# Kernel tuning notes

Hardware: AMD Instinct MI355X
Metric: run time of the kernel (lower is better)

The kernel has to match this reference:

```python
import jax, jax.numpy as jnp
import numpy as np

N_GRAPHS = 256
NEG_SLOPE = 0.2


def _add_self_loops(src, dst, edge_attr, n):
    # PyG fill_value='mean': self-loop edge_attr = per-node mean of incoming edge_attr
    sums = jax.ops.segment_sum(edge_attr, dst, num_segments=n)
    cnt = jax.ops.segment_sum(jnp.ones((dst.shape[0],), edge_attr.dtype), dst, num_segments=n)
    loop_attr = sums / jnp.maximum(cnt, 1.0)[:, None]
    loop = jnp.arange(n)
    src = jnp.concatenate([src, loop])
    dst = jnp.concatenate([dst, loop])
    ea = jnp.concatenate([edge_attr, loop_attr], axis=0)
    return src, dst, ea


def _segment_softmax(scores, seg, n):
    # scores: [E, H]; softmax over edges sharing the same target node
    m = jax.ops.segment_max(scores, seg, num_segments=n)
    ex = jnp.exp(scores - m[seg])
    s = jax.ops.segment_sum(ex, seg, num_segments=n)
    return ex / jnp.maximum(s[seg], 1e-16)


def gatv2_layer(x, src, dst, ea, w_l, w_r, w_e, att, b, heads, out_ch, concat):
    n = x.shape[0]
    x_l = (x @ w_l).reshape(n, heads, out_ch)  # source transform
    x_r = (x @ w_r).reshape(n, heads, out_ch)  # target transform
    e_f = (ea @ w_e).reshape(-1, heads, out_ch)
    m = x_l[src] + x_r[dst] + e_f                               # [E, H, C]
    score = jnp.einsum('ehc,hc->eh', jax.nn.leaky_relu(m, NEG_SLOPE), att)
    alpha = _segment_softmax(score, dst, n)                      # [E, H]
    out = jax.ops.segment_sum(alpha[:, :, None] * x_l[src], dst, num_segments=n)
    if concat:
        return out.reshape(n, heads * out_ch) + b
    return out.mean(axis=1) + b


def reference(x, edge_index, edge_attr, batch,
              w_l1, w_r1, w_e1, att1, b1,
              w_l2, w_r2, w_e2, att2, b2,
              w_fc, b_fc):
    n = x.shape[0]
    src, dst, ea = _add_self_loops(edge_index[0], edge_index[1], edge_attr, n)
    h = gatv2_layer(x, src, dst, ea, w_l1, w_r1, w_e1, att1, b1, heads=2, out_ch=32, concat=True)
    h = jax.nn.relu(h)
    h = gatv2_layer(h, src, dst, ea, w_l2, w_r2, w_e2, att2, b2, heads=1, out_ch=32, concat=False)
    h = jax.nn.relu(h)
    # global mean pool over graphs
    sums = jax.ops.segment_sum(h, batch, num_segments=N_GRAPHS)
    cnt = jax.ops.segment_sum(jnp.ones((n,), h.dtype), batch, num_segments=N_GRAPHS)
    pooled = sums / jnp.maximum(cnt, 1.0)[:, None]
    return pooled @ w_fc + b_fc


def setup_inputs() -> dict:
    key = jax.random.key(0)
    ks = jax.random.split(key, 20)
    N, E, IN, H, C, ED, OUT = 100000, 1600000, 128, 2, 32, 16, 32
    s = 0.05
    return {
        'x': jax.random.normal(ks[0], (N, IN), jnp.float32),
        'edge_index': jax.random.randint(ks[1], (2, E), 0, N, jnp.int32),
        'edge_attr': jax.random.normal(ks[2], (E, ED), jnp.float32),
        'batch': jnp.sort(jax.random.randint(ks[3], (N,), 0, 256, jnp.int32)),
        'w_l1': jax.random.normal(ks[4], (IN, H * C), jnp.float32) * s,
        'w_r1': jax.random.normal(ks[5], (IN, H * C), jnp.float32) * s,
        'w_e1': jax.random.normal(ks[6], (ED, H * C), jnp.float32) * s,
        'att1': jax.random.normal(ks[7], (H, C), jnp.float32) * s,
        'b1': jnp.zeros((H * C,), jnp.float32),
        'w_l2': jax.random.normal(ks[8], (H * C, C), jnp.float32) * s,
        'w_r2': jax.random.normal(ks[9], (H * C, C), jnp.float32) * s,
        'w_e2': jax.random.normal(ks[10], (ED, C), jnp.float32) * s,
        'att2': jax.random.normal(ks[11], (1, C), jnp.float32) * s,
        'b2': jnp.zeros((C,), jnp.float32),
        'w_fc': jax.random.normal(ks[12], (C, OUT), jnp.float32) * s,
        'b_fc': jnp.zeros((OUT,), jnp.float32),
    }
```

## Files before the change

kernel.cpp:

```cpp
#include <hip/hip_runtime.h>
#include <hip/hip_bf16.h>
#include <hip/hip_fp16.h>

#define NEG_SLOPE 0.2f
#define LOG2E 1.4426950408889634f
#define NROUNDS 8

typedef _Float16 h2v __attribute__((ext_vector_type(2)));
typedef __fp16 f16x2 __attribute__((ext_vector_type(2)));
union hu { h2v h; f16x2 f; unsigned int u; };

__device__ __forceinline__ float dot16h(uint4 u0, uint4 u1, const h2v* wh) {
  union { uint4 u; h2v h[4]; } a0, a1;
  a0.u = u0; a1.u = u1;
  float f0 = 0.f, f1 = 0.f;
  f0 = __builtin_amdgcn_fdot2(a0.h[0], wh[0], f0, false);
  f1 = __builtin_amdgcn_fdot2(a0.h[1], wh[1], f1, false);
  f0 = __builtin_amdgcn_fdot2(a0.h[2], wh[2], f0, false);
  f1 = __builtin_amdgcn_fdot2(a0.h[3], wh[3], f1, false);
  f0 = __builtin_amdgcn_fdot2(a1.h[0], wh[4], f0, false);
  f1 = __builtin_amdgcn_fdot2(a1.h[1], wh[5], f1, false);
  f0 = __builtin_amdgcn_fdot2(a1.h[2], wh[6], f0, false);
  f1 = __builtin_amdgcn_fdot2(a1.h[3], wh[7], f1, false);
  return f0 + f1;
}

__global__ void deg_count_k(const int* __restrict__ dstA, int* __restrict__ deg, int E) {
  int base = blockIdx.x * 1024 + threadIdx.x;
#pragma unroll
  for (int k = 0; k < 4; ++k) {
    int e = base + k * 256;
    if (e < E) atomicAdd(&deg[dstA[e]], 1);
  }
}

__global__ void scan1_k(const int* __restrict__ deg, int* __restrict__ rowptr,
                        int* __restrict__ aux, int N) {
  __shared__ int sh[256];
  int t = threadIdx.x, i = blockIdx.x * 256 + t;
  int v = (i < N) ? deg[i] : 0;
  sh[t] = v; __syncthreads();
  for (int off = 1; off < 256; off <<= 1) {
    int x = (t >= off) ? sh[t - off] : 0;
    __syncthreads();
    sh[t] += x;
    __syncthreads();
  }
  if (i < N) rowptr[i] = sh[t] - v;
  if (t == 255) aux[blockIdx.x] = sh[255];
}

__global__ void scan2_k(int* __restrict__ aux, int naux) {
  __shared__ int sh[512];
  int t = threadIdx.x;
  int v = (t < naux) ? aux[t] : 0;
  sh[t] = v; __syncthreads();
  for (int off = 1; off < 512; off <<= 1) {
    int x = (t >= off) ? sh[t - off] : 0;
    __syncthreads();
    sh[t] += x;
    __syncthreads();
  }
  if (t < naux) aux[t] = sh[t] - v;
}

__global__ void scan3_k(int* __restrict__ rowptr, int* __restrict__ cursor,
                        const int* __restrict__ aux, int N, int E) {
  int i = blockIdx.x * blockDim.x + threadIdx.x;
  if (i < N) {
    int r = rowptr[i] + aux[i >> 8];
    rowptr[i] = r;
    cursor[i] = r;
  } else if (i == N) {
    rowptr[N] = E;
  }
}

__global__ __launch_bounds__(256) void permute_ea_k(
    const int2* __restrict__ csr_se, const float* __restrict__ ea,
    unsigned int* __restrict__ ea_h_u, int E) {
  int gid = blockIdx.x * 256 + threadIdx.x;
  int slot = gid >> 3, sub = gid & 7;
  if (slot >= E) return;
  int eid = csr_se[slot].y;
  float2 v = ((const float2*)(ea + (size_t)eid * 16))[sub];
  hu p; p.f = __builtin_amdgcn_cvt_pkrtz(v.x, v.y);
  ea_h_u[(size_t)slot * 8 + sub] = p.u;
}

__global__ __launch_bounds__(256) void t1scat_k(
    const float* __restrict__ x, const float* __restrict__ wl, const float* __restrict__ wr,
    float* __restrict__ xl, float* __restrict__ xr, int N, int ntiles1,
    const int* __restrict__ srcA, const int* __restrict__ dstA,
    int* __restrict__ cursor, int2* __restrict__ csr_se, int E) {
  __shared__ unsigned int wS[64 * 128];
  __shared__ unsigned int xs[32 * 64];
  int t = threadIdx.x;
  if ((int)blockIdx.x >= ntiles1) {
    int sb = blockIdx.x - ntiles1;
    int round = sb & (NROUNDS - 1);
    int rb = sb >> 3;
    int nlo = (int)(((long long)round * N) / NROUNDS);
    int nhi = (int)(((long long)(round + 1) * N) / NROUNDS);
    int e4 = (rb * 256 + t) * 4;
    if (e4 + 3 < E) {
      int4 d4 = *(const int4*)(dstA + e4);
      int4 s4 = *(const int4*)(srcA + e4);
#pragma unroll
      for (int k = 0; k < 4; ++k) {
        int d = (&d4.x)[k];
        if (d >= nlo && d < nhi) {
          int pos = atomicAdd(&cursor[d], 1);
          csr_se[pos] = make_int2((&s4.x)[k], e4 + k);
        }
      }
    } else {
      for (int k = 0; k < 4; ++k) {
        int e = e4 + k;
        if (e < E) {
          int d = dstA[e];
          if (d >= nlo && d < nhi) {
            int pos = atomicAdd(&cursor[d], 1);
            csr_se[pos] = make_int2(srcA[e], e);
          }
        }
      }
    }
    return;
  }
  int tile = blockIdx.x;
  for (int i = t; i < 64 * 64; i += 256) {
    int kp = i >> 6, j = i & 63;
    hu pl, pr;
    pl.f = __builtin_amdgcn_cvt_pkrtz(wl[(2 * kp) * 64 + j], wl[(2 * kp + 1) * 64 + j]);
    pr.f = __builtin_amdgcn_cvt_pkrtz(wr[(2 * kp) * 64 + j], wr[(2 * kp + 1) * 64 + j]);
    wS[kp * 128 + j]      = pl.u;
    wS[kp * 128 + 64 + j] = pr.u;
  }
  {
    int base = tile << 5;
    const float4* x4 = (const float4*)x;
    for (int i = t; i < 1024; i += 256) {
      int node = base + (i >> 5);
      float4 v = {0.f, 0.f, 0.f, 0.f};
      if (node < N) v = x4[(size_t)node * 32 + (i & 31)];
      hu p0, p1;
      p0.f = __builtin_amdgcn_cvt_pkrtz(v.x, v.y);
      p1.f = __builtin_amdgcn_cvt_pkrtz(v.z, v.w);
      uint2* d = (uint2*)&xs[(i >> 5) * 64 + (i & 31) * 2];
      *d = make_uint2(p0.u, p1.u);
    }
    __syncthreads();
    int tc = t & 31;
    int tr = t >> 5;
    float4 acc0 = {0,0,0,0}, acc1 = {0,0,0,0}, acc2 = {0,0,0,0}, acc3 = {0,0,0,0};
    const unsigned int* xrow = &xs[tr * 4 * 64];
#pragma unroll 4
    for (int kp = 0; kp < 64; ++kp) {
      uint4 wu = *(const uint4*)&wS[kp * 128 + tc * 4];
      hu w0, w1, w2, w3, q0, q1, q2, q3;
      w0.u = wu.x; w1.u = wu.y; w2.u = wu.z; w3.u = wu.w;
      q0.u = xrow[kp]; q1.u = xrow[64 + kp]; q2.u = xrow[128 + kp]; q3.u = xrow[192 + kp];
      acc0.x = __builtin_amdgcn_fdot2(q0.h, w0.h, acc0.x, false);
      acc0.y = __builtin_amdgcn_fdot2(q0.h, w1.h, acc0.y, false);
      acc0.z = __builtin_amdgcn_fdot2(q0.h, w2.h, acc0.z, false);
      acc0.w = __builtin_amdgcn_fdot2(q0.h, w3.h, acc0.w, false);
      acc1.x = __builtin_amdgcn_fdot2(q1.h, w0.h, acc1.x, false);
      acc1.y = __builtin_amdgcn_fdot2(q1.h, w1.h, acc1.y, false);
      acc1.z = __builtin_amdgcn_fdot2(q1.h, w2.h, acc1.z, false);
      acc1.w = __builtin_amdgcn_fdot2(q1.h, w3.h, acc1.w, false);
      acc2.x = __builtin_amdgcn_fdot2(q2.h, w0.h, acc2.x, false);
      acc2.y = __builtin_amdgcn_fdot2(q2.h, w1.h, acc2.y, false);
      acc2.z = __builtin_amdgcn_fdot2(q2.h, w2.h, acc2.z, false);
      acc2.w = __builtin_amdgcn_fdot2(q2.h, w3.h, acc2.w, false);
      acc3.x = __builtin_amdgcn_fdot2(q3.h, w0.h, acc3.x, false);
      acc3.y = __builtin_amdgcn_fdot2(q3.h, w1.h, acc3.y, false);
      acc3.z = __builtin_amdgcn_fdot2(q3.h, w2.h, acc3.z, false);
      acc3.w = __builtin_amdgcn_fdot2(q3.h, w3.h, acc3.w, false);
    }
    float* dp = (tc < 16) ? xl : xr;
    int j4 = (tc & 15) * 4;
    int nb = base + tr * 4;
    if (nb + 0 < N) *(float4*)&dp[(size_t)(nb + 0) * 64 + j4] = acc0;
    if (nb + 1 < N) *(float4*)&dp[(size_t)(nb + 1) * 64 + j4] = acc1;
    if (nb + 2 < N) *(float4*)&dp[(size_t)(nb + 2) * 64 + j4] = acc2;
    if (nb + 3 < N) *(float4*)&dp[(size_t)(nb + 3) * 64 + j4] = acc3;
  }
}

__global__ __launch_bounds__(256) void transform2_k(
    const float* __restrict__ h, const float* __restrict__ wl, const float* __restrict__ wr,
    float* __restrict__ xl, float* __restrict__ xr, int N) {
  __shared__ unsigned int wS[32 * 64];
  __shared__ unsigned int xs[64 * 32];
  int t = threadIdx.x;
  for (int i = t; i < 32 * 32; i += 256) {
    int kp = i >> 5, j = i & 31;
    hu pl, pr;
    pl.f = __builtin_amdgcn_cvt_pkrtz(wl[(2 * kp) * 32 + j], wl[(2 * kp + 1) * 32 + j]);
    pr.f = __builtin_amdgcn_cvt_pkrtz(wr[(2 * kp) * 32 + j], wr[(2 * kp + 1) * 32 + j]);
    wS[kp * 64 + j]      = pl.u;
    wS[kp * 64 + 32 + j] = pr.u;
  }
  {
    int base = blockIdx.x << 6;
    const float4* h4 = (const float4*)h;
    for (int i = t; i < 1024; i += 256) {
      int node = base + (i >> 4);
      float4 v = {0.f, 0.f, 0.f, 0.f};
      if (node < N) v = h4[(size_t)node * 16 + (i & 15)];
      hu p0, p1;
      p0.f = __builtin_amdgcn_cvt_pkrtz(v.x, v.y);
      p1.f = __builtin_amdgcn_cvt_pkrtz(v.z, v.w);
      uint2* d = (uint2*)&xs[(i >> 4) * 32 + (i & 15) * 2];
      *d = make_uint2(p0.u, p1.u);
    }
    __syncthreads();
    int tc = t & 15;
    int tr = t >> 4;
    float4 acc0 = {0,0,0,0}, acc1 = {0,0,0,0}, acc2 = {0,0,0,0}, acc3 = {0,0,0,0};
    const unsigned int* xrow = &xs[tr * 4 * 32];
#pragma unroll 4
    for (int kp = 0; kp < 32; ++kp) {
      uint4 wu = *(const uint4*)&wS[kp * 64 + tc * 4];
      hu w0, w1, w2, w3, q0, q1, q2, q3;
      w0.u = wu.x; w1.u = wu.y; w2.u = wu.z; w3.u = wu.w;
      q0.u = xrow[kp]; q1.u = xrow[32 + kp]; q2.u = xrow[64 + kp]; q3.u = xrow[96 + kp];
      acc0.x = __builtin_amdgcn_fdot2(q0.h, w0.h, acc0.x, false);
      acc0.y = __builtin_amdgcn_fdot2(q0.h, w1.h, acc0.y, false);
      acc0.z = __builtin_amdgcn_fdot2(q0.h, w2.h, acc0.z, false);
      acc0.w = __builtin_amdgcn_fdot2(q0.h, w3.h, acc0.w, false);
      acc1.x = __builtin_amdgcn_fdot2(q1.h, w0.h, acc1.x, false);
      acc1.y = __builtin_amdgcn_fdot2(q1.h, w1.h, acc1.y, false);
      acc1.z = __builtin_amdgcn_fdot2(q1.h, w2.h, acc1.z, false);
      acc1.w = __builtin_amdgcn_fdot2(q1.h, w3.h, acc1.w, false);
      acc2.x = __builtin_amdgcn_fdot2(q2.h, w0.h, acc2.x, false);
      acc2.y = __builtin_amdgcn_fdot2(q2.h, w1.h, acc2.y, false);
      acc2.z = __builtin_amdgcn_fdot2(q2.h, w2.h, acc2.z, false);
      acc2.w = __builtin_amdgcn_fdot2(q2.h, w3.h, acc2.w, false);
      acc3.x = __builtin_amdgcn_fdot2(q3.h, w0.h, acc3.x, false);
      acc3.y = __builtin_amdgcn_fdot2(q3.h, w1.h, acc3.y, false);
      acc3.z = __builtin_amdgcn_fdot2(q3.h, w2.h, acc3.z, false);
      acc3.w = __builtin_amdgcn_fdot2(q3.h, w3.h, acc3.w, false);
    }
    float* dp = (tc < 8) ? xl : xr;
    int j4 = (tc & 7) * 4;
    int nb = base + tr * 4;
    if (nb + 0 < N) *(float4*)&dp[(size_t)(nb + 0) * 32 + j4] = acc0;
    if (nb + 1 < N) *(float4*)&dp[(size_t)(nb + 1) * 32 + j4] = acc1;
    if (nb + 2 < N) *(float4*)&dp[(size_t)(nb + 2) * 32 + j4] = acc2;
    if (nb + 3 < N) *(float4*)&dp[(size_t)(nb + 3) * 32 + j4] = acc3;
  }
}

__global__ __launch_bounds__(256) void gat1_k(
    const int* __restrict__ rowptr, const int2* __restrict__ csr_se,
    const uint4* __restrict__ ea_h, const float* __restrict__ we,
    const float* __restrict__ att, const float* __restrict__ b,
    const float* __restrict__ xl, const float* __restrict__ xr,
    float* __restrict__ h, int N) {
  int t = threadIdx.x;
  int lane = t & 63;
  h2v wh[8];
#pragma unroll
  for (int k = 0; k < 8; ++k) {
    wh[k].x = (_Float16)we[(2 * k) * 64 + lane];
    wh[k].y = (_Float16)we[(2 * k + 1) * 64 + lane];
  }
  float att_r = att[lane] * LOG2E;
  float b_r = b[lane];
  int wid = (blockIdx.x * blockDim.x + t) >> 6;
  int n0 = wid * 4;
  for (int jj = 0; jj < 4; ++jj) {
    int n = n0 + jj;
    if (n >= N) break;
    float xr_v = xr[(size_t)n * 64 + lane];
    float xl_s = xl[(size_t)n * 64 + lane];
    float num = 0.f, den = 0.f, efsum = 0.f;
    int rs = __builtin_amdgcn_readfirstlane(rowptr[n]);
    int re = __builtin_amdgcn_readfirstlane(rowptr[n + 1]);
    for (int base = rs; base < re; base += 64) {
      int cnt = min(64, re - base);
      int s_l = 0;
      if (lane < cnt) s_l = csr_se[base + lane].x;
      int i = 0;
      for (; i + 3 < cnt; i += 4) {
        int sa = __builtin_amdgcn_readlane(s_l, i);
        int sb = __builtin_amdgcn_readlane(s_l, i + 1);
        int sc_ = __builtin_amdgcn_readlane(s_l, i + 2);
        int sd = __builtin_amdgcn_readlane(s_l, i + 3);
        float xa = (xl + (size_t)sa * 64)[lane];
        float xb = (xl + (size_t)sb * 64)[lane];
        float xc = (xl + (size_t)sc_ * 64)[lane];
        float xd = (xl + (size_t)sd * 64)[lane];
        const uint4* ep = ea_h + (size_t)(base + i) * 2;
        uint4 u0 = ep[0], u1 = ep[1], u2 = ep[2], u3 = ep[3];
        uint4 u4 = ep[4], u5 = ep[5], u6 = ep[6], u7 = ep[7];
        float fa = dot16h(u0, u1, wh);
        float fb = dot16h(u2, u3, wh);
        float fc = dot16h(u4, u5, wh);
        float fd = dot16h(u6, u7, wh);
        float ma = xa + xr_v + fa; ma = fmaxf(ma, NEG_SLOPE * ma);
        float mb = xb + xr_v + fb; mb = fmaxf(mb, NEG_SLOPE * mb);
        float mc = xc + xr_v + fc; mc = fmaxf(mc, NEG_SLOPE * mc);
        float md = xd + xr_v + fd; md = fmaxf(md, NEG_SLOPE * md);
        float ta = ma * att_r, tb = mb * att_r, tc2 = mc * att_r, td = md * att_r;
#pragma unroll
        for (int off = 1; off < 32; off <<= 1) {
          ta  += __shfl_xor(ta, off);
          tb  += __shfl_xor(tb, off);
          tc2 += __shfl_xor(tc2, off);
          td  += __shfl_xor(td, off);
        }
        float ga = __builtin_amdgcn_exp2f(ta);
        float gb = __builtin_amdgcn_exp2f(tb);
        float gc = __builtin_amdgcn_exp2f(tc2);
        float gd = __builtin_amdgcn_exp2f(td);
        num += ga * xa + gb * xb + gc * xc + gd * xd;
        den += ga + gb + gc + gd;
        efsum += fa + fb + fc + fd;
      }
      for (; i < cnt; ++i) {
        int sa = __builtin_amdgcn_readlane(s_l, i);
        float xa = (xl + (size_t)sa * 64)[lane];
        const uint4* ep = ea_h + (size_t)(base + i) * 2;
        uint4 u0 = ep[0], u1 = ep[1];
        float fa = dot16h(u0, u1, wh);
        float ma = xa + xr_v + fa; ma = fmaxf(ma, NEG_SLOPE * ma);
        float ta = ma * att_r;
#pragma unroll
        for (int off = 1; off < 32; off <<= 1) ta += __shfl_xor(ta, off);
        float ga = __builtin_amdgcn_exp2f(ta);
        num += ga * xa;
        den += ga;
        efsum += fa;
      }
    }
    int deg = re - rs;
    float ef_self = efsum * __builtin_amdgcn_rcpf(fmaxf((float)deg, 1.f));
    float mm = xl_s + xr_v + ef_self;
    mm = fmaxf(mm, NEG_SLOPE * mm);
    float s2 = mm * att_r;
#pragma unroll
    for (int off = 1; off < 32; off <<= 1) s2 += __shfl_xor(s2, off);
    float e2 = __builtin_amdgcn_exp2f(s2);
    num += e2 * xl_s;
    den += e2;
    h[(size_t)n * 64 + lane] = fmaxf(num * __builtin_amdgcn_rcpf(fmaxf(den, 1e-16f)) + b_r, 0.f);
  }
}

__global__ __launch_bounds__(256) void gat2_k(
    const int* __restrict__ rowptr, const int2* __restrict__ csr_se,
    const uint4* __restrict__ ea_h, const float* __restrict__ we,
    const float* __restrict__ att, const float* __restrict__ b,
    const float* __restrict__ xl, const float* __restrict__ xr,
    float* __restrict__ h, int N) {
  int t = threadIdx.x;
  int lane = t & 63;
  int c = lane & 31;
  int half = lane >> 5;
  int hbase = lane & 32;
  h2v wh[8];
#pragma unroll
  for (int k = 0; k < 8; ++k) {
    wh[k].x = (_Float16)we[(2 * k) * 32 + c];
    wh[k].y = (_Float16)we[(2 * k + 1) * 32 + c];
  }
  float att_r = att[c] * LOG2E;
  float b_r = b[c];
  int wid = (blockIdx.x * blockDim.x + t) >> 6;
  int p0 = wid * 4;
  for (int jj = 0; jj < 4; ++jj) {
    int p = p0 + jj;
    if (p * 2 >= N) break;
    int n = p * 2 + half;
    if (n >= N) continue;
    float xr_v = xr[(size_t)n * 32 + c];
    float xl_s = xl[(size_t)n * 32 + c];
    float num = 0.f, den = 0.f, efsum = 0.f;
    int rs = rowptr[n], re = rowptr[n + 1];
    for (int base = rs; base < re; base += 32) {
      int cnt = min(32, re - base);
      int s_l = 0;
      if (c < cnt) s_l = csr_se[base + c].x;
      int i = 0;
      for (; i + 1 < cnt; i += 2) {
        int sa = __shfl(s_l, hbase + i), sb = __shfl(s_l, hbase + i + 1);
        float xa = xl[(size_t)sa * 32 + c];
        float xb = xl[(size_t)sb * 32 + c];
        const uint4* epa = ea_h + (size_t)(base + i) * 2;
        uint4 u0 = epa[0], u1 = epa[1], u2 = epa[2], u3 = epa[3];
        float fa = dot16h(u0, u1, wh);
        float fb = dot16h(u2, u3, wh);
        float ma = xa + xr_v + fa; ma = fmaxf(ma, NEG_SLOPE * ma);
        float mb = xb + xr_v + fb; mb = fmaxf(mb, NEG_SLOPE * mb);
        float ta = ma * att_r, tb = mb * att_r;
#pragma unroll
        for (int off = 1; off < 32; off <<= 1) {
          ta += __shfl_xor(ta, off);
          tb += __shfl_xor(tb, off);
        }
        float ga = __builtin_amdgcn_exp2f(ta), gb = __builtin_amdgcn_exp2f(tb);
        num += ga * xa + gb * xb;
        den += ga + gb;
        efsum += fa + fb;
      }
      if (i < cnt) {
        int sa = __shfl(s_l, hbase + i);
        float xa = xl[(size_t)sa * 32 + c];
        const uint4* epa = ea_h + (size_t)(base + i) * 2;
        uint4 u0 = epa[0], u1 = epa[1];
        float fa = dot16h(u0, u1, wh);
        float ma = xa + xr_v + fa; ma = fmaxf(ma, NEG_SLOPE * ma);
        float ta = ma * att_r;
#pragma unroll
        for (int off = 1; off < 32; off <<= 1) ta += __shfl_xor(ta, off);
        float ga = __builtin_amdgcn_exp2f(ta);
        num += ga * xa;
        den += ga;
        efsum += fa;
      }
    }
    int deg = re - rs;
    float ef_self = efsum * __builtin_amdgcn_rcpf(fmaxf((float)deg, 1.f));
    float mm = xl_s + xr_v + ef_self;
    mm = fmaxf(mm, NEG_SLOPE * mm);
    float s2 = mm * att_r;
#pragma unroll
    for (int off = 1; off < 32; off <<= 1) s2 += __shfl_xor(s2, off);
    float e2 = __builtin_amdgcn_exp2f(s2);
    num += e2 * xl_s;
    den += e2;
    h[(size_t)n * 32 + c] = fmaxf(num * __builtin_amdgcn_rcpf(fmaxf(den, 1e-16f)) + b_r, 0.f);
  }
}

__global__ __launch_bounds__(256) void pool_fc_k(
    const float* __restrict__ h, const int* __restrict__ batch,
    const float* __restrict__ wfc, const float* __restrict__ bfc,
    float* __restrict__ out, int N) {
  int g = blockIdx.x;
  __shared__ int srange[2];
  __shared__ float part[8][32];
  int t = threadIdx.x;
  if (t < 2) {
    int key = g + t;
    int lo = 0, hi = N;
    while (lo < hi) { int mid = (lo + hi) >> 1; if (batch[mid] < key) lo = mid + 1; else hi = mid; }
    srange[t] = lo;
  }
  __syncthreads();
  int rs = srange[0], re = srange[1];
  int c = t & 31, sub = t >> 5;
  float acc = 0.f;
  for (int n = rs + sub; n < re; n += 8) acc += h[(size_t)n * 32 + c];
  part[sub][c] = acc;
  __syncthreads();
  if (sub == 0) {
    float s = part[0][c];
#pragma unroll
    for (int i = 1; i < 8; ++i) s += part[i][c];
    part[0][c] = s / fmaxf((float)(re - rs), 1.f);
  }
  __syncthreads();
  if (sub == 0) {
    float a = 0.f;
#pragma unroll
    for (int k = 0; k < 32; ++k) a += part[0][k] * wfc[k * 32 + c];
    out[g * 32 + c] = a + bfc[c];
  }
}

extern "C" void kernel_launch(void* const* d_in, const int* in_sizes, int n_in,
                              void* d_out, int out_size, void* d_ws, size_t ws_size,
                              hipStream_t stream) {
  const float* x   = (const float*)d_in[0];
  const int*   ei  = (const int*)d_in[1];
  const float* ea  = (const float*)d_in[2];
  const int*   bat = (const int*)d_in[3];
  const float* wl1 = (const float*)d_in[4];
  const float* wr1 = (const float*)d_in[5];
  const float* we1 = (const float*)d_in[6];
  const float* at1 = (const float*)d_in[7];
  const float* b1  = (const float*)d_in[8];
  const float* wl2 = (const float*)d_in[9];
  const float* wr2 = (const float*)d_in[10];
  const float* we2 = (const float*)d_in[11];
  const float* at2 = (const float*)d_in[12];
  const float* b2  = (const float*)d_in[13];
  const float* wfc = (const float*)d_in[14];
  const float* bfc = (const float*)d_in[15];

  const int N = in_sizes[0] / 128;
  const int E = in_sizes[1] / 2;
  const int G = 256;
  const int* srcA = ei;
  const int* dstA = ei + E;

  uint4* ea_h   = (uint4*)d_ws;
  float* xl1    = (float*)(ea_h + (size_t)E * 2);
  float* xr1    = xl1 + (size_t)N * 64;
  int*   deg    = (int*)(xr1 + (size_t)N * 64);
  int*   rowptr = deg + N;
  int*   cursor = rowptr + (N + 1);
  int*   aux    = cursor + N;
  int2*  csr_se = (int2*)(aux + 512);
  float* h1     = xr1;
  float* xl2    = xl1;
  float* xr2    = xl1 + (size_t)N * 32;
  float* h2     = xr2;

  const int naux = (N + 255) / 256;
  const int ntiles1 = (N + 31) / 32;
  const int perRound = (E + 1023) / 1024;

  (void)hipMemsetAsync(deg, 0, (size_t)N * sizeof(int), stream);
  deg_count_k<<<(E + 1023) / 1024, 256, 0, stream>>>(dstA, deg, E);
  scan1_k<<<naux, 256, 0, stream>>>(deg, rowptr, aux, N);
  scan2_k<<<1, 512, 0, stream>>>(aux, naux);
  scan3_k<<<(N + 256) / 256, 256, 0, stream>>>(rowptr, cursor, aux, N, E);

  t1scat_k<<<ntiles1 + NROUNDS * perRound, 256, 0, stream>>>(
      x, wl1, wr1, xl1, xr1, N, ntiles1,
      srcA, dstA, cursor, csr_se, E);
  {
    long long thr = (long long)E * 8;
    permute_ea_k<<<(int)((thr + 255) / 256), 256, 0, stream>>>(csr_se, ea,
                                                               (unsigned int*)ea_h, E);
  }

  {
    int blocks1 = (N + 15) / 16;
    gat1_k<<<blocks1, 256, 0, stream>>>(rowptr, csr_se, ea_h, we1, at1, b1,
                                        xl1, xr1, h1, N);
  }

  transform2_k<<<(N + 63) / 64, 256, 0, stream>>>(h1, wl2, wr2, xl2, xr2, N);
  {
    int P = (N + 1) / 2;
    int blocks2 = (P + 15) / 16;
    gat2_k<<<blocks2, 256, 0, stream>>>(rowptr, csr_se, ea_h, we2, at2, b2,
                                        xl2, xr2, h2, N);
  }

  pool_fc_k<<<G, 256, 0, stream>>>(h2, bat, wfc, bfc, (float*)d_out, N);
}
```

Baseline: 464.1 us.

## Co-schedule layer-1 transform with degree counting instead of the scatter pass

The layer-1 node transform (x@W_l, x@W_r) now shares a launch with the atomic degree-count blocks rather than with the CSR scatter blocks. The scatter becomes its own standalone kernel launched after the scan. The intent is to hide the short, atomic-bound degree count behind the compute-heavy transform tiles. The trade-off is that the scatter, previously overlapped with the transform, now runs alone. The scatter blocks are light (no shared memory), which may give them higher occupancy when run separately, while the fused degree blocks carry the transform's large shared-memory footprint.

Result: no change. 467.9 us (+0.8%).

```diff
diff --git a/kernel.cpp b/kernel.cpp
--- a/kernel.cpp
+++ b/kernel.cpp
@@ -25,110 +25,23 @@
   return f0 + f1;
 }
 
-__global__ void deg_count_k(const int* __restrict__ dstA, int* __restrict__ deg, int E) {
-  int base = blockIdx.x * 1024 + threadIdx.x;
-#pragma unroll
-  for (int k = 0; k < 4; ++k) {
-    int e = base + k * 256;
-    if (e < E) atomicAdd(&deg[dstA[e]], 1);
-  }
-}
-
-__global__ void scan1_k(const int* __restrict__ deg, int* __restrict__ rowptr,
-                        int* __restrict__ aux, int N) {
-  __shared__ int sh[256];
-  int t = threadIdx.x, i = blockIdx.x * 256 + t;
-  int v = (i < N) ? deg[i] : 0;
-  sh[t] = v; __syncthreads();
-  for (int off = 1; off < 256; off <<= 1) {
-    int x = (t >= off) ? sh[t - off] : 0;
-    __syncthreads();
-    sh[t] += x;
-    __syncthreads();
-  }
-  if (i < N) rowptr[i] = sh[t] - v;
-  if (t == 255) aux[blockIdx.x] = sh[255];
-}
-
-__global__ void scan2_k(int* __restrict__ aux, int naux) {
-  __shared__ int sh[512];
-  int t = threadIdx.x;
-  int v = (t < naux) ? aux[t] : 0;
-  sh[t] = v; __syncthreads();
-  for (int off = 1; off < 512; off <<= 1) {
-    int x = (t >= off) ? sh[t - off] : 0;
-    __syncthreads();
-    sh[t] += x;
-    __syncthreads();
-  }
-  if (t < naux) aux[t] = sh[t] - v;
-}
-
-__global__ void scan3_k(int* __restrict__ rowptr, int* __restrict__ cursor,
-                        const int* __restrict__ aux, int N, int E) {
-  int i = blockIdx.x * blockDim.x + threadIdx.x;
-  if (i < N) {
-    int r = rowptr[i] + aux[i >> 8];
-    rowptr[i] = r;
-    cursor[i] = r;
-  } else if (i == N) {
-    rowptr[N] = E;
-  }
-}
-
-__global__ __launch_bounds__(256) void permute_ea_k(
-    const int2* __restrict__ csr_se, const float* __restrict__ ea,
-    unsigned int* __restrict__ ea_h_u, int E) {
-  int gid = blockIdx.x * 256 + threadIdx.x;
-  int slot = gid >> 3, sub = gid & 7;
-  if (slot >= E) return;
-  int eid = csr_se[slot].y;
-  float2 v = ((const float2*)(ea + (size_t)eid * 16))[sub];
-  hu p; p.f = __builtin_amdgcn_cvt_pkrtz(v.x, v.y);
-  ea_h_u[(size_t)slot * 8 + sub] = p.u;
-}
-
-__global__ __launch_bounds__(256) void t1scat_k(
+__global__ __launch_bounds__(256) void t1deg_k(
     const float* __restrict__ x, const float* __restrict__ wl, const float* __restrict__ wr,
-    float* __restrict__ xl, float* __restrict__ xr, int N, int ntiles1,
-    const int* __restrict__ srcA, const int* __restrict__ dstA,
-    int* __restrict__ cursor, int2* __restrict__ csr_se, int E) {
+    float* __restrict__ xl, float* __restrict__ xr, int N,
+    const int* __restrict__ dstA, int* __restrict__ deg, int E, int degBlocks) {
   __shared__ unsigned int wS[64 * 128];
   __shared__ unsigned int xs[32 * 64];
   int t = threadIdx.x;
-  if ((int)blockIdx.x >= ntiles1) {
-    int sb = blockIdx.x - ntiles1;
-    int round = sb & (NROUNDS - 1);
-    int rb = sb >> 3;
-    int nlo = (int)(((long long)round * N) / NROUNDS);
-    int nhi = (int)(((long long)(round + 1) * N) / NROUNDS);
-    int e4 = (rb * 256 + t) * 4;
-    if (e4 + 3 < E) {
-      int4 d4 = *(const int4*)(dstA + e4);
-      int4 s4 = *(const int4*)(srcA + e4);
-#pragma unroll
-      for (int k = 0; k < 4; ++k) {
-        int d = (&d4.x)[k];
-        if (d >= nlo && d < nhi) {
-          int pos = atomicAdd(&cursor[d], 1);
-          csr_se[pos] = make_int2((&s4.x)[k], e4 + k);
-        }
-      }
-    } else {
-      for (int k = 0; k < 4; ++k) {
-        int e = e4 + k;
-        if (e < E) {
-          int d = dstA[e];
-          if (d >= nlo && d < nhi) {
-            int pos = atomicAdd(&cursor[d], 1);
-            csr_se[pos] = make_int2(srcA[e], e);
-          }
-        }
-      }
+  if ((int)blockIdx.x < degBlocks) {
+    int base = blockIdx.x * 1024 + t;
+#pragma unroll
+    for (int k = 0; k < 4; ++k) {
+      int e = base + k * 256;
+      if (e < E) atomicAdd(&deg[dstA[e]], 1);
     }
     return;
   }
-  int tile = blockIdx.x;
+  int tile = blockIdx.x - degBlocks;
   for (int i = t; i < 64 * 64; i += 256) {
     int kp = i >> 6, j = i & 63;
     hu pl, pr;
@@ -186,6 +99,93 @@
     if (nb + 2 < N) *(float4*)&dp[(size_t)(nb + 2) * 64 + j4] = acc2;
     if (nb + 3 < N) *(float4*)&dp[(size_t)(nb + 3) * 64 + j4] = acc3;
   }
+}
+
+__global__ void scan1_k(const int* __restrict__ deg, int* __restrict__ rowptr,
+                        int* __restrict__ aux, int N) {
+  __shared__ int sh[256];
+  int t = threadIdx.x, i = blockIdx.x * 256 + t;
+  int v = (i < N) ? deg[i] : 0;
+  sh[t] = v; __syncthreads();
+  for (int off = 1; off < 256; off <<= 1) {
+    int x = (t >= off) ? sh[t - off] : 0;
+    __syncthreads();
+    sh[t] += x;
+    __syncthreads();
+  }
+  if (i < N) rowptr[i] = sh[t] - v;
+  if (t == 255) aux[blockIdx.x] = sh[255];
+}
+
+__global__ void scan2_k(int* __restrict__ aux, int naux) {
+  __shared__ int sh[512];
+  int t = threadIdx.x;
+  int v = (t < naux) ? aux[t] : 0;
+  sh[t] = v; __syncthreads();
+  for (int off = 1; off < 512; off <<= 1) {
+    int x = (t >= off) ? sh[t - off] : 0;
+    __syncthreads();
+    sh[t] += x;
+    __syncthreads();
+  }
+  if (t < naux) aux[t] = sh[t] - v;
+}
+
+__global__ void scan3_k(int* __restrict__ rowptr, int* __restrict__ cursor,
+                        const int* __restrict__ aux, int N, int E) {
+  int i = blockIdx.x * blockDim.x + threadIdx.x;
+  if (i < N) {
+    int r = rowptr[i] + aux[i >> 8];
+    rowptr[i] = r;
+    cursor[i] = r;
+  } else if (i == N) {
+    rowptr[N] = E;
+  }
+}
+
+__global__ __launch_bounds__(256) void scat_k(
+    const int* __restrict__ srcA, const int* __restrict__ dstA,
+    int* __restrict__ cursor, int2* __restrict__ csr_se, int N, int E) {
+  int round = blockIdx.x & (NROUNDS - 1);
+  int rb = blockIdx.x >> 3;
+  int nlo = (int)(((long long)round * N) / NROUNDS);
+  int nhi = (int)(((long long)(round + 1) * N) / NROUNDS);
+  int e4 = (rb * 256 + threadIdx.x) * 4;
+  if (e4 + 3 < E) {
+    int4 d4 = *(const int4*)(dstA + e4);
+    int4 s4 = *(const int4*)(srcA + e4);
+#pragma unroll
+    for (int k = 0; k < 4; ++k) {
+      int d = (&d4.x)[k];
+      if (d >= nlo && d < nhi) {
+        int pos = atomicAdd(&cursor[d], 1);
+        csr_se[pos] = make_int2((&s4.x)[k], e4 + k);
+      }
+    }
+  } else {
+    for (int k = 0; k < 4; ++k) {
+      int e = e4 + k;
+      if (e < E) {
+        int d = dstA[e];
+        if (d >= nlo && d < nhi) {
+          int pos = atomicAdd(&cursor[d], 1);
+          csr_se[pos] = make_int2(srcA[e], e);
+        }
+      }
+    }
+  }
+}
+
+__global__ __launch_bounds__(256) void permute_ea_k(
+    const int2* __restrict__ csr_se, const float* __restrict__ ea,
+    unsigned int* __restrict__ ea_h_u, int E) {
+  int gid = blockIdx.x * 256 + threadIdx.x;
+  int slot = gid >> 3, sub = gid & 7;
+  if (slot >= E) return;
+  int eid = csr_se[slot].y;
+  float2 v = ((const float2*)(ea + (size_t)eid * 16))[sub];
+  hu p; p.f = __builtin_amdgcn_cvt_pkrtz(v.x, v.y);
+  ea_h_u[(size_t)slot * 8 + sub] = p.u;
 }
 
 __global__ __launch_bounds__(256) void transform2_k(
@@ -513,17 +513,17 @@
 
   const int naux = (N + 255) / 256;
   const int ntiles1 = (N + 31) / 32;
+  const int degBlocks = (E + 1023) / 1024;
   const int perRound = (E + 1023) / 1024;
 
   (void)hipMemsetAsync(deg, 0, (size_t)N * sizeof(int), stream);
-  deg_count_k<<<(E + 1023) / 1024, 256, 0, stream>>>(dstA, deg, E);
+  t1deg_k<<<degBlocks + ntiles1, 256, 0, stream>>>(x, wl1, wr1, xl1, xr1, N,
+                                                   dstA, deg, E, degBlocks);
   scan1_k<<<naux, 256, 0, stream>>>(deg, rowptr, aux, N);
   scan2_k<<<1, 512, 0, stream>>>(aux, naux);
   scan3_k<<<(N + 256) / 256, 256, 0, stream>>>(rowptr, cursor, aux, N, E);
 
-  t1scat_k<<<ntiles1 + NROUNDS * perRound, 256, 0, stream>>>(
-      x, wl1, wr1, xl1, xr1, N, ntiles1,
-      srcA, dstA, cursor, csr_se, E);
+  scat_k<<<NROUNDS * perRound, 256, 0, stream>>>(srcA, dstA, cursor, csr_se, N, E);
   {
     long long thr = (long long)E * 8;
     permute_ea_k<<<(int)((thr + 255) / 256), 256, 0, stream>>>(csr_se, ea,
```
